# Performance work log

Measured on AMD Instinct MI355X. Metric: run time of the kernel, lower is better.

## Reference

```python
import jax, jax.numpy as jnp
import numpy as np

B, L, D = 8, 4096, 1024   # batch, max words, sent_dim
S, SENT_LEN = 255, 16     # sentences per sample, words per sentence (255*16=4080)
START_BOUND = 1           # leading zero-pad region, as in the torch module


def setup_inputs() -> dict:
    key = jax.random.key(0)
    k1, k2, k3, k4 = jax.random.split(key, 4)
    words_emb = jax.random.normal(k1, (B, L, D), jnp.float32)
    sents_emb = jax.random.normal(k2, (B, S, D), jnp.float32)
    # nn.Linear(2D, D): weight [D, 2D], bias [D]
    W1_w = jax.random.normal(k3, (D, 2 * D), jnp.float32) / np.sqrt(2 * D)
    W1_b = jax.random.normal(k4, (D,), jnp.float32) * 0.01
    # sentence-index-per-word map; -1 marks the zero-padded regions
    sm = -np.ones((B, L), np.int32)
    idx = np.repeat(np.arange(S, dtype=np.int32), SENT_LEN)  # [S*SENT_LEN]
    sm[:, START_BOUND:START_BOUND + S * SENT_LEN] = idx
    sent_map = jnp.asarray(sm)
    return {"words_emb": words_emb, "sents_emb": sents_emb,
            "W1_w": W1_w, "W1_b": W1_b, "sent_map": sent_map}


def reference(words_emb, sents_emb, W1_w, W1_b, sent_map):
    # Expand sentence embeddings to word positions via gather; zero outside spans.
    valid = sent_map >= 0                                    # [B, L]
    safe_idx = jnp.clip(sent_map, 0)                         # [B, L]
    gathered = jnp.take_along_axis(sents_emb, safe_idx[..., None], axis=1)  # [B, L, D]
    sents_state_flat = jnp.where(valid[..., None], gathered, 0.0)
    # concat word + sentence features, then Linear + ReLU
    x = jnp.concatenate([words_emb, sents_state_flat], axis=-1)  # [B, L, 2D]
    return jax.nn.relu(jnp.einsum('ble,de->bld', x, W1_w) + W1_b)
```

## Files before the change

### kernel.cpp

```cpp
#include <hip/hip_runtime.h>
#include <stdint.h>

constexpr int kB = 8;
constexpr int kL = 4096;
constexpr int kD = 1024;
constexpr int kS = 255;
constexpr int kM = kB * kL;
constexpr int kK = 2 * kD;
constexpr int kN = kD;

#define TILE_M 128
#define TILE_N 128
#define TILE_K 32

typedef __bf16 bf16x8 __attribute__((ext_vector_type(8)));
typedef float  f32x4  __attribute__((ext_vector_type(4)));

constexpr size_t WS_WORDS = 0;
constexpr size_t WS_SENTS = WS_WORDS + (size_t)kM * kD * 2;
constexpr size_t WS_W     = WS_SENTS + (size_t)kB * kS * kD * 2;
constexpr size_t WS_ZP    = WS_W + (size_t)kN * kK * 2;
constexpr size_t WS_NEED  = WS_ZP + 3072;

__device__ __forceinline__ uint32_t pk_bf16x2(float a, float b) {
    uint32_t ua = __float_as_uint(a) + 0x8000u;
    uint32_t ub = __float_as_uint(b) + 0x8000u;
    return __builtin_amdgcn_perm(ub, ua, 0x07060302u);
}

__device__ __forceinline__ void async16(const void* g, void* l) {
    __builtin_amdgcn_global_load_lds(
        (const __attribute__((address_space(1))) uint32_t*)g,
        (__attribute__((address_space(3))) uint32_t*)l, 16, 0, 0);
}

__global__ __launch_bounds__(256)
void cvt_prepass(const float4* __restrict__ words, const float4* __restrict__ sents,
                 const float4* __restrict__ W,
                 uint2* __restrict__ wordsB, uint2* __restrict__ sentsB,
                 uint2* __restrict__ WB, uint32_t* __restrict__ zp)
{
    constexpr size_t NW = (size_t)kM * kD / 4;
    constexpr size_t NS = (size_t)kB * kS * kD / 4;
    constexpr size_t NT = NW + NS + (size_t)kN * kK / 4;
    if (blockIdx.x == 0) {
        for (int t = threadIdx.x; t < 768; t += 256) zp[t] = 0u;
    }
    size_t i = (size_t)blockIdx.x * 256 + threadIdx.x;
    if (i >= NT) return;
    float4 v; uint2* dst;
    if (i < NW)            { v = words[i];            dst = wordsB + i; }
    else if (i < NW + NS)  { v = sents[i - NW];       dst = sentsB + (i - NW); }
    else                   { v = W[i - NW - NS];      dst = WB + (i - NW - NS); }
    uint2 o;
    o.x = pk_bf16x2(v.x, v.y);
    o.y = pk_bf16x2(v.z, v.w);
    *dst = o;
}

__global__ __launch_bounds__(256)
void wsib_gemm_bf(const uint8_t* __restrict__ wordsB,
                  const uint8_t* __restrict__ sentsB,
                  const uint8_t* __restrict__ WB,
                  const float*   __restrict__ bias,
                  const int*     __restrict__ smap,
                  const uint8_t* __restrict__ zp,
                  float* __restrict__ out)
{
    __shared__ uint8_t AsmB[TILE_M * TILE_K * 2];
    __shared__ uint8_t BsmB[TILE_N * TILE_K * 2];

    const int tid = threadIdx.x;
    const int nT  = blockIdx.x;
    const int mT  = blockIdx.y;

    const int r1 = tid >> 2;
    const int ch = (tid & 3) * 16;
    const int m1 = mT * TILE_M + r1, m2 = m1 + 64;
    const int b1 = m1 >> 12;
    const uint8_t* wA1 = wordsB + (size_t)m1 * (kD * 2) + ch;
    const uint8_t* wA2 = wordsB + (size_t)m2 * (kD * 2) + ch;
    const int s1 = smap[m1], s2 = smap[m2];
    const uint8_t* sA1 = (s1 >= 0) ? sentsB + ((size_t)(b1 * kS + s1)) * (kD * 2) + ch : zp + ch;
    const uint8_t* sA2 = (s2 >= 0) ? sentsB + ((size_t)(b1 * kS + s2)) * (kD * 2) + ch : zp + ch;
    const uint8_t* wB1 = WB + (size_t)(nT * TILE_N + r1) * (kK * 2) + ch;
    const uint8_t* wB2 = wB1 + (size_t)64 * (kK * 2);

    const int w = tid >> 6;
    uint8_t* ldsA = AsmB + w * 1024;
    uint8_t* ldsB = BsmB + w * 1024;

    const int lane = tid & 63;
    const int wm   = (w & 1) * 64;
    const int wn   = (w >> 1) * 64;
    const int fr   = lane & 15;
    const int quad = lane >> 4;

    f32x4 acc[4][4];
    #pragma unroll
    for (int i = 0; i < 4; ++i)
        #pragma unroll
        for (int j = 0; j < 4; ++j)
            acc[i][j] = (f32x4){0.f, 0.f, 0.f, 0.f};

    auto kstep = [&](const uint8_t* a1, const uint8_t* a2,
                     const uint8_t* b1p, const uint8_t* b2p) {
        __syncthreads();
        async16(a1,  ldsA);
        async16(a2,  ldsA + 4096);
        async16(b1p, ldsB);
        async16(b2p, ldsB + 4096);
        __syncthreads();

        bf16x8 af[4], bfv[4];
        #pragma unroll
        for (int mi = 0; mi < 4; ++mi)
            af[mi] = *(const bf16x8*)&AsmB[(wm + mi * 16 + fr) * 64 + quad * 16];
        #pragma unroll
        for (int ni = 0; ni < 4; ++ni)
            bfv[ni] = *(const bf16x8*)&BsmB[(wn + ni * 16 + fr) * 64 + quad * 16];

        #pragma unroll
        for (int mi = 0; mi < 4; ++mi)
            #pragma unroll
            for (int ni = 0; ni < 4; ++ni)
                acc[mi][ni] = __builtin_amdgcn_mfma_f32_16x16x32_bf16(
                    af[mi], bfv[ni], acc[mi][ni], 0, 0, 0);
    };

    for (int k0 = 0; k0 < kD; k0 += TILE_K)
        kstep(wA1 + k0 * 2, wA2 + k0 * 2, wB1 + k0 * 2, wB2 + k0 * 2);
    for (int k0 = 0; k0 < kD; k0 += TILE_K)
        kstep(sA1 + k0 * 2, sA2 + k0 * 2, wB1 + (kD + k0) * 2, wB2 + (kD + k0) * 2);

    const int rowBase = mT * TILE_M + wm;
    const int colBase = nT * TILE_N + wn;
    float bv[4];
    #pragma unroll
    for (int ni = 0; ni < 4; ++ni) bv[ni] = bias[colBase + ni * 16 + fr];

    #pragma unroll
    for (int mi = 0; mi < 4; ++mi) {
        #pragma unroll
        for (int ni = 0; ni < 4; ++ni) {
            const int col = colBase + ni * 16 + fr;
            #pragma unroll
            for (int r = 0; r < 4; ++r) {
                const int row = rowBase + mi * 16 + quad * 4 + r;
                float v = acc[mi][ni][r] + bv[ni];
                out[(size_t)row * kN + col] = fmaxf(v, 0.f);
            }
        }
    }
}

#define LDS_STRIDE 20
__global__ __launch_bounds__(256)
void wsib_gemm_fb(const float* __restrict__ words, const float* __restrict__ sents,
                  const float* __restrict__ W, const float* __restrict__ bias,
                  const int* __restrict__ smap, float* __restrict__ out)
{
    __shared__ uint32_t Asm[TILE_M * LDS_STRIDE];
    __shared__ uint32_t Bsm[TILE_N * LDS_STRIDE];
    const int tid = threadIdx.x, nT = blockIdx.x, mT = blockIdx.y;
    const int sRow = tid >> 1, half = tid & 1;
    const int mRow = mT * TILE_M + sRow, bIdx = mRow >> 12;
    const float* wsrc = words + (size_t)mRow * kD + half * 16;
    const int sidx = smap[mRow];
    const float* ssrc = (sidx >= 0) ? sents + ((size_t)bIdx * kS + sidx) * kD + half * 16 : nullptr;
    const float* bsrc = W + (size_t)(nT * TILE_N + sRow) * kK + half * 16;
    uint32_t* adst = &Asm[sRow * LDS_STRIDE + half * 8];
    uint32_t* bdst = &Bsm[sRow * LDS_STRIDE + half * 8];
    const int lane = tid & 63, wv = tid >> 6;
    const int wm = (wv & 1) * 64, wn = (wv >> 1) * 64;
    const int fr = lane & 15, quad = lane >> 4;
    f32x4 acc[4][4];
    #pragma unroll
    for (int i = 0; i < 4; ++i)
        #pragma unroll
        for (int j = 0; j < 4; ++j) acc[i][j] = (f32x4){0.f, 0.f, 0.f, 0.f};
    float4 ra[4], rb[4];
    {
        const float4* pa = (const float4*)wsrc; const float4* pb = (const float4*)bsrc;
        #pragma unroll
        for (int i = 0; i < 4; ++i) { ra[i] = pa[i]; rb[i] = pb[i]; }
    }
    for (int k0 = 0; k0 < kK; k0 += TILE_K) {
        uint32_t pa[8], pb[8];
        #pragma unroll
        for (int i = 0; i < 4; ++i) {
            pa[2*i] = pk_bf16x2(ra[i].x, ra[i].y); pa[2*i+1] = pk_bf16x2(ra[i].z, ra[i].w);
            pb[2*i] = pk_bf16x2(rb[i].x, rb[i].y); pb[2*i+1] = pk_bf16x2(rb[i].z, rb[i].w);
        }
        __syncthreads();
        ((uint4*)adst)[0] = make_uint4(pa[0], pa[1], pa[2], pa[3]);
        ((uint4*)adst)[1] = make_uint4(pa[4], pa[5], pa[6], pa[7]);
        ((uint4*)bdst)[0] = make_uint4(pb[0], pb[1], pb[2], pb[3]);
        ((uint4*)bdst)[1] = make_uint4(pb[4], pb[5], pb[6], pb[7]);
        __syncthreads();
        const int k1 = k0 + TILE_K;
        if (k1 < kK) {
            const float* asrc = (k1 < kD) ? (wsrc + k1) : (ssrc ? (ssrc + (k1 - kD)) : nullptr);
            if (asrc) { const float4* p = (const float4*)asrc;
                #pragma unroll
                for (int i = 0; i < 4; ++i) ra[i] = p[i];
            } else {
                #pragma unroll
                for (int i = 0; i < 4; ++i) ra[i] = make_float4(0.f, 0.f, 0.f, 0.f);
            }
            const float4* p = (const float4*)(bsrc + k1);
            #pragma unroll
            for (int i = 0; i < 4; ++i) rb[i] = p[i];
        }
        bf16x8 af[4], bfv[4];
        #pragma unroll
        for (int mi = 0; mi < 4; ++mi)
            af[mi] = *(const bf16x8*)&Asm[(wm + mi * 16 + fr) * LDS_STRIDE + quad * 4];
        #pragma unroll
        for (int ni = 0; ni < 4; ++ni)
            bfv[ni] = *(const bf16x8*)&Bsm[(wn + ni * 16 + fr) * LDS_STRIDE + quad * 4];
        #pragma unroll
        for (int mi = 0; mi < 4; ++mi)
            #pragma unroll
            for (int ni = 0; ni < 4; ++ni)
                acc[mi][ni] = __builtin_amdgcn_mfma_f32_16x16x32_bf16(af[mi], bfv[ni], acc[mi][ni], 0, 0, 0);
    }
    const int rowBase = mT * TILE_M + wm, colBase = nT * TILE_N + wn;
    float bv[4];
    #pragma unroll
    for (int ni = 0; ni < 4; ++ni) bv[ni] = bias[colBase + ni * 16 + fr];
    #pragma unroll
    for (int mi = 0; mi < 4; ++mi)
        #pragma unroll
        for (int ni = 0; ni < 4; ++ni) {
            const int col = colBase + ni * 16 + fr;
            #pragma unroll
            for (int r = 0; r < 4; ++r) {
                const int row = rowBase + mi * 16 + quad * 4 + r;
                out[(size_t)row * kN + col] = fmaxf(acc[mi][ni][r] + bv[ni], 0.f);
            }
        }
}

extern "C" void kernel_launch(void* const* d_in, const int* in_sizes, int n_in,
                              void* d_out, int out_size, void* d_ws, size_t ws_size,
                              hipStream_t stream) {
    const float* words = (const float*)d_in[0];
    const float* sents = (const float*)d_in[1];
    const float* W     = (const float*)d_in[2];
    const float* bias  = (const float*)d_in[3];
    const int*   smap  = (const int*)d_in[4];
    float* out = (float*)d_out;

    if (ws_size >= WS_NEED) {
        uint8_t* ws = (uint8_t*)d_ws;
        uint2* wordsB = (uint2*)(ws + WS_WORDS);
        uint2* sentsB = (uint2*)(ws + WS_SENTS);
        uint2* WB     = (uint2*)(ws + WS_W);
        uint32_t* zp  = (uint32_t*)(ws + WS_ZP);
        constexpr size_t totalV4 = ((size_t)kM * kD + (size_t)kB * kS * kD + (size_t)kN * kK) / 4;
        const int cvtBlocks = (int)((totalV4 + 255) / 256);
        cvt_prepass<<<cvtBlocks, 256, 0, stream>>>(
            (const float4*)words, (const float4*)sents, (const float4*)W,
            wordsB, sentsB, WB, zp);
        dim3 grid(kN / TILE_N, kM / TILE_M);
        wsib_gemm_bf<<<grid, 256, 0, stream>>>(
            (const uint8_t*)wordsB, (const uint8_t*)sentsB, (const uint8_t*)WB,
            bias, smap, (const uint8_t*)zp, out);
    } else {
        dim3 grid(kN / TILE_N, kM / TILE_M);
        wsib_gemm_fb<<<grid, 256, 0, stream>>>(words, sents, W, bias, smap, out);
    }
}
```

Baseline: 418.9 us.

## Rewrite bf16 GEMM with 256x256 tiles, triple-buffered async LDS and swizzle

Replaces the 128x128, 256-thread GEMM with a 256x256, 512-thread kernel. It triple-buffers global-to-LDS async loads with explicit vmcnt waits and raw barriers, XOR-swizzles LDS rows to avoid bank conflicts, and interleaves the MFMA halves with prefetch issue under raised wave priority. The conversion prepass now runs as a grid-stride loop that writes 16-byte outputs. The aim is higher arithmetic intensity and hiding load latency behind compute, at the cost of more registers and LDS (96KB) per block and more fragile hand-placed wait counts.

```diff
diff --git a/kernel.cpp b/kernel.cpp
--- a/kernel.cpp
+++ b/kernel.cpp
@@ -9,10 +9,6 @@
 constexpr int kK = 2 * kD;
 constexpr int kN = kD;
 
-#define TILE_M 128
-#define TILE_N 128
-#define TILE_K 32
-
 typedef __bf16 bf16x8 __attribute__((ext_vector_type(8)));
 typedef float  f32x4  __attribute__((ext_vector_type(4)));
 
@@ -34,32 +30,47 @@
         (__attribute__((address_space(3))) uint32_t*)l, 16, 0, 0);
 }
 
+#define WAITVM(n)  asm volatile("s_waitcnt vmcnt(" #n ")" ::: "memory")
+#define WAITLGKM0  asm volatile("s_waitcnt lgkmcnt(0)" ::: "memory")
+
+__device__ __forceinline__ void blockbar() {
+    asm volatile("" ::: "memory");
+    __builtin_amdgcn_s_barrier();
+    asm volatile("" ::: "memory");
+}
+
 __global__ __launch_bounds__(256)
-void cvt_prepass(const float4* __restrict__ words, const float4* __restrict__ sents,
-                 const float4* __restrict__ W,
-                 uint2* __restrict__ wordsB, uint2* __restrict__ sentsB,
-                 uint2* __restrict__ WB, uint32_t* __restrict__ zp)
+void cvt_prepass2(const float4* __restrict__ words, const float4* __restrict__ sents,
+                  const float4* __restrict__ W,
+                  uint4* __restrict__ wordsB, uint4* __restrict__ sentsB,
+                  uint4* __restrict__ WB, uint32_t* __restrict__ zp)
 {
-    constexpr size_t NW = (size_t)kM * kD / 4;
-    constexpr size_t NS = (size_t)kB * kS * kD / 4;
-    constexpr size_t NT = NW + NS + (size_t)kN * kK / 4;
+    constexpr size_t NW8 = (size_t)kM * kD / 8;
+    constexpr size_t NS8 = (size_t)kB * kS * kD / 8;
+    constexpr size_t NB8 = (size_t)kN * kK / 8;
+    constexpr size_t NT8 = NW8 + NS8 + NB8;
     if (blockIdx.x == 0) {
         for (int t = threadIdx.x; t < 768; t += 256) zp[t] = 0u;
     }
-    size_t i = (size_t)blockIdx.x * 256 + threadIdx.x;
-    if (i >= NT) return;
-    float4 v; uint2* dst;
-    if (i < NW)            { v = words[i];            dst = wordsB + i; }
-    else if (i < NW + NS)  { v = sents[i - NW];       dst = sentsB + (i - NW); }
-    else                   { v = W[i - NW - NS];      dst = WB + (i - NW - NS); }
-    uint2 o;
-    o.x = pk_bf16x2(v.x, v.y);
-    o.y = pk_bf16x2(v.z, v.w);
-    *dst = o;
-}
-
-__global__ __launch_bounds__(256)
-void wsib_gemm_bf(const uint8_t* __restrict__ wordsB,
+    const size_t stride = (size_t)gridDim.x * blockDim.x;
+    for (size_t i = (size_t)blockIdx.x * blockDim.x + threadIdx.x; i < NT8; i += stride) {
+        const float4* src; uint4* dst; size_t j;
+        if (i < NW8)            { src = words; dst = wordsB; j = i; }
+        else if (i < NW8 + NS8) { src = sents; dst = sentsB; j = i - NW8; }
+        else                    { src = W;     dst = WB;     j = i - NW8 - NS8; }
+        float4 a  = src[2 * j];
+        float4 b2 = src[2 * j + 1];
+        uint4 o;
+        o.x = pk_bf16x2(a.x,  a.y);
+        o.y = pk_bf16x2(a.z,  a.w);
+        o.z = pk_bf16x2(b2.x, b2.y);
+        o.w = pk_bf16x2(b2.z, b2.w);
+        dst[j] = o;
+    }
+}
+
+__global__ __launch_bounds__(512, 2)
+void wsib_gemm_v2(const uint8_t* __restrict__ wordsB,
                   const uint8_t* __restrict__ sentsB,
                   const uint8_t* __restrict__ WB,
                   const float*   __restrict__ bias,
@@ -67,93 +78,141 @@
                   const uint8_t* __restrict__ zp,
                   float* __restrict__ out)
 {
-    __shared__ uint8_t AsmB[TILE_M * TILE_K * 2];
-    __shared__ uint8_t BsmB[TILE_N * TILE_K * 2];
-
-    const int tid = threadIdx.x;
-    const int nT  = blockIdx.x;
-    const int mT  = blockIdx.y;
-
-    const int r1 = tid >> 2;
-    const int ch = (tid & 3) * 16;
-    const int m1 = mT * TILE_M + r1, m2 = m1 + 64;
-    const int b1 = m1 >> 12;
-    const uint8_t* wA1 = wordsB + (size_t)m1 * (kD * 2) + ch;
-    const uint8_t* wA2 = wordsB + (size_t)m2 * (kD * 2) + ch;
-    const int s1 = smap[m1], s2 = smap[m2];
-    const uint8_t* sA1 = (s1 >= 0) ? sentsB + ((size_t)(b1 * kS + s1)) * (kD * 2) + ch : zp + ch;
-    const uint8_t* sA2 = (s2 >= 0) ? sentsB + ((size_t)(b1 * kS + s2)) * (kD * 2) + ch : zp + ch;
-    const uint8_t* wB1 = WB + (size_t)(nT * TILE_N + r1) * (kK * 2) + ch;
-    const uint8_t* wB2 = wB1 + (size_t)64 * (kK * 2);
-
-    const int w = tid >> 6;
-    uint8_t* ldsA = AsmB + w * 1024;
-    uint8_t* ldsB = BsmB + w * 1024;
-
+    __shared__ uint8_t lds[3][2][16384];
+
+    const int tid  = threadIdx.x;
+    const int w    = tid >> 6;
     const int lane = tid & 63;
-    const int wm   = (w & 1) * 64;
-    const int wn   = (w >> 1) * 64;
-    const int fr   = lane & 15;
-    const int quad = lane >> 4;
-
-    f32x4 acc[4][4];
-    #pragma unroll
-    for (int i = 0; i < 4; ++i)
-        #pragma unroll
-        for (int j = 0; j < 4; ++j)
-            acc[i][j] = (f32x4){0.f, 0.f, 0.f, 0.f};
-
-    auto kstep = [&](const uint8_t* a1, const uint8_t* a2,
-                     const uint8_t* b1p, const uint8_t* b2p) {
-        __syncthreads();
-        async16(a1,  ldsA);
-        async16(a2,  ldsA + 4096);
-        async16(b1p, ldsB);
-        async16(b2p, ldsB + 4096);
-        __syncthreads();
-
-        bf16x8 af[4], bfv[4];
-        #pragma unroll
-        for (int mi = 0; mi < 4; ++mi)
-            af[mi] = *(const bf16x8*)&AsmB[(wm + mi * 16 + fr) * 64 + quad * 16];
+    const int nT = blockIdx.x;
+    const int mT = blockIdx.y;
+
+    const int wm = (w >> 2) * 128;
+    const int wn = (w & 3) * 64;
+    const int fr = lane & 15, quad = lane >> 4;
+
+    float bv[4];
+    #pragma unroll
+    for (int ni = 0; ni < 4; ++ni) bv[ni] = bias[nT * 256 + wn + ni * 16 + fr];
+
+    const int lrow = lane >> 2;
+    const int cph  = lane & 3;
+    const int lc   = cph ^ (lrow & 3) ^ ((lrow >> 2) & 3);
+    const int rloc0 = w * 32 + lrow;
+    const int rloc1 = rloc0 + 16;
+    const int gA0 = mT * 256 + rloc0, gA1 = mT * 256 + rloc1;
+    const uint8_t* aw0 = wordsB + (size_t)gA0 * 2048 + lc * 16;
+    const uint8_t* aw1 = wordsB + (size_t)gA1 * 2048 + lc * 16;
+    const int bIdx = gA0 >> 12;
+    const int s0 = smap[gA0], s1 = smap[gA1];
+    const uint8_t* as0 = (s0 >= 0) ? sentsB + (size_t)(bIdx * kS + s0) * 2048 + lc * 16
+                                   : zp + lc * 16;
+    const uint8_t* as1 = (s1 >= 0) ? sentsB + (size_t)(bIdx * kS + s1) * 2048 + lc * 16
+                                   : zp + lc * 16;
+    const uint8_t* wb0 = WB + (size_t)(nT * 256 + rloc0) * 4096 + lc * 16;
+    const uint8_t* wb1 = WB + (size_t)(nT * 256 + rloc1) * 4096 + lc * 16;
+
+    const int pc   = quad ^ (fr & 3) ^ ((fr >> 2) & 3);
+    const int offA = (wm + fr) * 64 + pc * 16;
+    const int offB = (wn + fr) * 64 + pc * 16;
+
+    f32x4 acc[8][4];
+    #pragma unroll
+    for (int i = 0; i < 8; ++i)
+        #pragma unroll
+        for (int j = 0; j < 4; ++j) acc[i][j] = (f32x4){0.f, 0.f, 0.f, 0.f};
+
+    auto srcA0 = [&](int t) { return (t < 32) ? aw0 + (t << 6) : as0 + ((t - 32) << 6); };
+    auto srcA1 = [&](int t) { return (t < 32) ? aw1 + (t << 6) : as1 + ((t - 32) << 6); };
+
+    {
+        uint8_t* A0 = lds[0][0]; uint8_t* B0 = lds[0][1];
+        async16(srcA0(0), A0 + w * 2048);
+        async16(srcA1(0), A0 + w * 2048 + 1024);
+        async16(wb0,      B0 + w * 2048);
+        async16(wb1,      B0 + w * 2048 + 1024);
+        uint8_t* A1 = lds[1][0]; uint8_t* B1 = lds[1][1];
+        async16(srcA0(1), A1 + w * 2048);
+        async16(srcA1(1), A1 + w * 2048 + 1024);
+        async16(wb0 + 64, B1 + w * 2048);
+        async16(wb1 + 64, B1 + w * 2048 + 1024);
+    }
+
+    int bufR = 0;
+    #pragma unroll 1
+    for (int t = 0; t < 64; ++t) {
+        uint8_t* ldsAr = lds[bufR][0];
+        uint8_t* ldsBr = lds[bufR][1];
+        const int bufS = (bufR == 0) ? 2 : bufR - 1;
+        uint8_t* ldsAs = lds[bufS][0];
+        uint8_t* ldsBs = lds[bufS][1];
+        const int tS = t + 2;
+
+        WAITLGKM0;
+        if (t < 63) { WAITVM(4); } else { WAITVM(0); }
+        blockbar();
+
+        bf16x8 bf[4];
         #pragma unroll
         for (int ni = 0; ni < 4; ++ni)
-            bfv[ni] = *(const bf16x8*)&BsmB[(wn + ni * 16 + fr) * 64 + quad * 16];
-
+            bf[ni] = *(const bf16x8*)(ldsBr + offB + ni * 1024);
+        bf16x8 af[4];
+        #pragma unroll
+        for (int mi = 0; mi < 4; ++mi)
+            af[mi] = *(const bf16x8*)(ldsAr + offA + mi * 1024);
+        if (tS < 64) {
+            async16(srcA0(tS), ldsAs + w * 2048);
+            async16(srcA1(tS), ldsAs + w * 2048 + 1024);
+        }
+        blockbar();
+        __builtin_amdgcn_s_setprio(1);
         #pragma unroll
         for (int mi = 0; mi < 4; ++mi)
             #pragma unroll
             for (int ni = 0; ni < 4; ++ni)
                 acc[mi][ni] = __builtin_amdgcn_mfma_f32_16x16x32_bf16(
-                    af[mi], bfv[ni], acc[mi][ni], 0, 0, 0);
-    };
-
-    for (int k0 = 0; k0 < kD; k0 += TILE_K)
-        kstep(wA1 + k0 * 2, wA2 + k0 * 2, wB1 + k0 * 2, wB2 + k0 * 2);
-    for (int k0 = 0; k0 < kD; k0 += TILE_K)
-        kstep(sA1 + k0 * 2, sA2 + k0 * 2, wB1 + (kD + k0) * 2, wB2 + (kD + k0) * 2);
-
-    const int rowBase = mT * TILE_M + wm;
-    const int colBase = nT * TILE_N + wn;
-    float bv[4];
-    #pragma unroll
-    for (int ni = 0; ni < 4; ++ni) bv[ni] = bias[colBase + ni * 16 + fr];
-
-    #pragma unroll
-    for (int mi = 0; mi < 4; ++mi) {
+                    af[mi], bf[ni], acc[mi][ni], 0, 0, 0);
+        __builtin_amdgcn_s_setprio(0);
+
+        bf16x8 ag[4];
+        #pragma unroll
+        for (int mi = 0; mi < 4; ++mi)
+            ag[mi] = *(const bf16x8*)(ldsAr + offA + (mi + 4) * 1024);
+        if (tS < 64) {
+            async16(wb0 + (tS << 6), ldsBs + w * 2048);
+            async16(wb1 + (tS << 6), ldsBs + w * 2048 + 1024);
+        }
+        blockbar();
+        __builtin_amdgcn_s_setprio(1);
+        #pragma unroll
+        for (int mi = 0; mi < 4; ++mi)
+            #pragma unroll
+            for (int ni = 0; ni < 4; ++ni)
+                acc[mi + 4][ni] = __builtin_amdgcn_mfma_f32_16x16x32_bf16(
+                    ag[mi], bf[ni], acc[mi + 4][ni], 0, 0, 0);
+        __builtin_amdgcn_s_setprio(0);
+
+        bufR = (bufR == 2) ? 0 : bufR + 1;
+    }
+
+    const int rowBase = mT * 256 + wm + quad * 4;
+    const int colBase = nT * 256 + wn + fr;
+    #pragma unroll
+    for (int mi = 0; mi < 8; ++mi) {
         #pragma unroll
         for (int ni = 0; ni < 4; ++ni) {
-            const int col = colBase + ni * 16 + fr;
+            const int col = colBase + ni * 16;
             #pragma unroll
             for (int r = 0; r < 4; ++r) {
-                const int row = rowBase + mi * 16 + quad * 4 + r;
-                float v = acc[mi][ni][r] + bv[ni];
-                out[(size_t)row * kN + col] = fmaxf(v, 0.f);
+                const int row = rowBase + mi * 16 + r;
+                out[(size_t)row * kN + col] = fmaxf(acc[mi][ni][r] + bv[ni], 0.f);
             }
         }
     }
 }
 
+#define TILE_M 128
+#define TILE_N 128
+#define TILE_K 32
 #define LDS_STRIDE 20
 __global__ __launch_bounds__(256)
 void wsib_gemm_fb(const float* __restrict__ words, const float* __restrict__ sents,
@@ -254,17 +313,15 @@
 
     if (ws_size >= WS_NEED) {
         uint8_t* ws = (uint8_t*)d_ws;
-        uint2* wordsB = (uint2*)(ws + WS_WORDS);
-        uint2* sentsB = (uint2*)(ws + WS_SENTS);
-        uint2* WB     = (uint2*)(ws + WS_W);
+        uint4* wordsB = (uint4*)(ws + WS_WORDS);
+        uint4* sentsB = (uint4*)(ws + WS_SENTS);
+        uint4* WB     = (uint4*)(ws + WS_W);
         uint32_t* zp  = (uint32_t*)(ws + WS_ZP);
-        constexpr size_t totalV4 = ((size_t)kM * kD + (size_t)kB * kS * kD + (size_t)kN * kK) / 4;
-        const int cvtBlocks = (int)((totalV4 + 255) / 256);
-        cvt_prepass<<<cvtBlocks, 256, 0, stream>>>(
+        cvt_prepass2<<<2048, 256, 0, stream>>>(
             (const float4*)words, (const float4*)sents, (const float4*)W,
             wordsB, sentsB, WB, zp);
-        dim3 grid(kN / TILE_N, kM / TILE_M);
-        wsib_gemm_bf<<<grid, 256, 0, stream>>>(
+        dim3 grid(kN / 256, kM / 256);
+        wsib_gemm_v2<<<grid, 512, 0, stream>>>(
             (const uint8_t*)wordsB, (const uint8_t*)sentsB, (const uint8_t*)WB,
             bias, smap, (const uint8_t*)zp, out);
     } else {
```

Measured after the change: 373.4 us. -10.9%, faster.
